# Kernel tuning notes

Hardware: AMD Instinct MI355X
Metric: run time of the kernel (lower is better)

The kernel has to match this reference:

```python
import jax, jax.numpy as jnp
import numpy as np

N_NODES = 50000
N_EDGES = 600000
D_EMB = 128
D_HID = 128
N_HEADS = 4
N_MABS = 7  # ISAB0(mab0,mab1), ISAB1(mab0,mab1), PMA, SAB, SAB
B, S = 16, 512
PROTO = 5


def setup_inputs() -> dict:
    key = jax.random.key(0)
    ks = jax.random.split(key, 24)
    nrm = lambda k, shape, s=0.05: jax.random.normal(k, shape, jnp.float32) * s
    node_embed = nrm(ks[0], (N_NODES + 1, D_EMB), 1.0).at[0].set(0.0)  # padding_idx=0
    return {
        'node_ids': jax.random.randint(ks[1], (B, S), 0, N_NODES),
        'edge_idx': jax.random.randint(ks[2], (2, N_EDGES), 0, N_NODES),
        'edge_attr': jax.random.normal(ks[3], (N_EDGES,), jnp.float32),
        'node_embed': node_embed,
        'lin_W': nrm(ks[4], (D_EMB, D_HID)), 'lin_b': jnp.zeros((D_HID,), jnp.float32),
        'gat_W': nrm(ks[5], (D_HID, D_HID)),
        'gat_att_src': nrm(ks[6], (D_HID,)), 'gat_att_dst': nrm(ks[7], (D_HID,)),
        'gat_bias': jnp.zeros((D_HID,), jnp.float32),
        'mab_Wq': nrm(ks[8], (N_MABS, D_HID, D_HID)), 'mab_bq': jnp.zeros((N_MABS, D_HID), jnp.float32),
        'mab_Wk': nrm(ks[9], (N_MABS, D_HID, D_HID)), 'mab_bk': jnp.zeros((N_MABS, D_HID), jnp.float32),
        'mab_Wv': nrm(ks[10], (N_MABS, D_HID, D_HID)), 'mab_bv': jnp.zeros((N_MABS, D_HID), jnp.float32),
        'mab_Wo': nrm(ks[11], (N_MABS, D_HID, D_HID)), 'mab_bo': jnp.zeros((N_MABS, D_HID), jnp.float32),
        'isab_I': nrm(ks[12], (2, 1, D_HID), 1.0),   # 2 ISAB blocks, num_inds=1
        'pma_S': nrm(ks[13], (1, D_HID), 1.0),       # num_outputs=1 seed
        'dec_W': nrm(ks[14], (D_HID, D_HID)), 'dec_b': jnp.zeros((D_HID,), jnp.float32),
        'prototypes': nrm(ks[15], (1, PROTO, D_HID), 1.0),
    }


def mab(Q, K, Wq, bq, Wk, bk, Wv, bv, Wo, bo):
    # Set-transformer MAB, ln=False; residual uses projected Q; scale by sqrt(full dim)
    D = Q.shape[-1]
    h, d = N_HEADS, D // N_HEADS
    Qp = Q @ Wq + bq
    Kp = K @ Wk + bk
    Vp = K @ Wv + bv
    sh = lambda x: x.reshape(x.shape[0], x.shape[1], h, d).transpose(0, 2, 1, 3)
    A = jax.nn.softmax(jnp.einsum('bhqd,bhkd->bhqk', sh(Qp), sh(Kp)) / np.sqrt(D).astype(np.float32))
    O = sh(Qp) + jnp.einsum('bhqk,bhkd->bhqd', A, sh(Vp))
    O = O.transpose(0, 2, 1, 3).reshape(Q.shape[0], Q.shape[1], D)
    return O + jax.nn.relu(O @ Wo + bo)


def reference(node_ids, edge_idx, edge_attr, node_embed, lin_W, lin_b, gat_W,
              gat_att_src, gat_att_dst, gat_bias, mab_Wq, mab_bq, mab_Wk, mab_bk,
              mab_Wv, mab_bv, mab_Wo, mab_bo, isab_I, pma_S, dec_W, dec_b, prototypes):
    # embed all nodes then linear
    x = node_embed[jnp.arange(N_NODES)] @ lin_W + lin_b          # [N, H]
    # GATConv (1 head, negative_slope=0.2, add_self_loops=True; edge_attr unused)
    loops = jnp.arange(N_NODES)
    src = jnp.concatenate([edge_idx[0], loops])
    dst = jnp.concatenate([edge_idx[1], loops])
    xw = x @ gat_W                                               # [N, H]
    a_s = xw @ gat_att_src                                       # [N]
    a_d = xw @ gat_att_dst
    e = jax.nn.leaky_relu(a_s[src] + a_d[dst], 0.2)              # [E+N]
    m = jax.ops.segment_max(e, dst, num_segments=N_NODES)
    ex = jnp.exp(e - m[dst])
    den = jax.ops.segment_sum(ex, dst, num_segments=N_NODES)
    coef = ex / den[dst]
    x = jax.ops.segment_sum(coef[:, None] * xw[src], dst, num_segments=N_NODES) + gat_bias
    # gather per-sample node sets
    X = x[node_ids]                                              # [B, S, H]
    b = X.shape[0]
    def mb(i, Q, K):
        return mab(Q, K, mab_Wq[i], mab_bq[i], mab_Wk[i], mab_bk[i],
                   mab_Wv[i], mab_bv[i], mab_Wo[i], mab_bo[i])
    # encoder: 2 ISAB blocks (num_inds=1)
    for i in range(2):
        Hb = mb(2 * i, jnp.broadcast_to(isab_I[i][None], (b, 1, D_HID)), X)
        X = mb(2 * i + 1, X, Hb)
    # decoder: PMA -> SAB -> SAB -> Linear
    X = mb(4, jnp.broadcast_to(pma_S[None], (b, 1, D_HID)), X)
    X = mb(5, X, X)
    X = mb(6, X, X)
    X = X @ dec_W + dec_b                                        # [B, 1, H]
    proto = jnp.broadcast_to(prototypes, (b, PROTO, D_HID))
    return jnp.concatenate([X, proto], axis=1)                   # [B, 6, H]
```

## Files before the change

kernel.cpp:

```cpp
#include <hip/hip_runtime.h>
#include <math.h>

#define N_NODES 50000
#define N_EDGES 600000
#define BATCH 16
#define SEQ 512
#define NROWS (BATCH*SEQ)
#define N_ITEMS (N_EDGES + N_NODES)

#define OFF_XW     0L
#define OFF_X      (OFF_XW + 6400000L)
#define OFF_ACC    (OFF_X + 1048576L)
#define OFF_AS     (OFF_ACC + 1048576L)
#define OFF_AD     (OFF_AS + 50000L)
#define OFF_WC     (OFF_AD + 50000L)
#define OFF_BC     (OFF_WC + 16384L)
#define OFF_QP     (OFF_BC + 128L)
#define OFF_WKH    (OFF_QP + 384L)
#define OFF_CKH    (OFF_WKH + 1536L)
#define OFF_VPOD   (OFF_CKH + 16L)
#define OFF_MASK   (OFF_VPOD + 2048L)
#define OFF_DEG    (OFF_MASK + 50000L)
#define OFF_FILL   (OFF_DEG + 8192L)
#define OFF_CNT    (OFF_FILL + 8192L)
#define ZERO_BYTES ((50000L + 8192L + 8192L + 4L) * 4L)
#define OFF_MAP    (OFF_CNT + 4L)
#define OFF_INV    (OFF_MAP + 50000L)
#define OFF_ROWPTR (OFF_INV + 8192L)
#define OFF_COL    (OFF_ROWPTR + 8194L)

__global__ __launch_bounds__(256) void prep_kernel(
    const float* __restrict__ lin_W, const float* __restrict__ lin_b,
    const float* __restrict__ gat_W,
    const float* __restrict__ mab_Wq, const float* __restrict__ mab_bq,
    const float* __restrict__ isab_I, const float* __restrict__ pma_S,
    float* __restrict__ Wc, float* __restrict__ bc, float* __restrict__ qp)
{
    int t = blockIdx.x * 256 + threadIdx.x;
    if (t < 16384) {
        int i = t >> 7, j = t & 127;
        float s = 0.f;
        for (int k = 0; k < 128; ++k) s += lin_W[i*128 + k] * gat_W[k*128 + j];
        Wc[t] = s;
    } else if (t < 16512) {
        int j = t - 16384;
        float s = 0.f;
        for (int k = 0; k < 128; ++k) s += lin_b[k] * gat_W[k*128 + j];
        bc[j] = s;
    } else if (t < 16896) {
        int u = t - 16512;
        int m = u >> 7, c = u & 127;
        int mi = m * 2;
        const float* vec = (m == 0) ? isab_I : (m == 1 ? isab_I + 128 : pma_S);
        float s = mab_bq[mi*128 + c];
        for (int k = 0; k < 128; ++k) s += vec[k] * mab_Wq[mi*16384 + k*128 + c];
        qp[u] = s;
    }
}

__global__ __launch_bounds__(256) void prep2_kernel(
    const float* __restrict__ mab_Wk, const float* __restrict__ mab_bk,
    const float* __restrict__ qp, float* __restrict__ wkh, float* __restrict__ ckh)
{
    int t = blockIdx.x * 256 + threadIdx.x;
    if (t < 1536) {
        int m = t >> 9;
        int h = (t >> 7) & 3;
        int j = t & 127;
        int mi = m * 2;
        const float* Wk = mab_Wk + mi*16384 + j*128 + h*32;
        const float* q  = qp + m*128 + h*32;
        float s = 0.f;
        #pragma unroll
        for (int d = 0; d < 32; ++d) s += Wk[d] * q[d];
        wkh[t] = s;
    } else if (t < 1548) {
        int u = t - 1536;
        int m = u >> 2, h = u & 3;
        int mi = m * 2;
        const float* bk = mab_bk + mi*128 + h*32;
        const float* q  = qp + m*128 + h*32;
        float s = 0.f;
        #pragma unroll
        for (int d = 0; d < 32; ++d) s += bk[d] * q[d];
        ckh[u] = s;
    }
}

__global__ __launch_bounds__(256) void gemm0_kernel(
    const float* __restrict__ Xin, const float* __restrict__ W1,
    const float* __restrict__ b1, float* __restrict__ out1)
{
    __shared__ float Xs[16][128];
    int t = threadIdx.x;
    long row0 = (long)blockIdx.x * 16;
    #pragma unroll
    for (int i = 0; i < 8; ++i) {
        int idx = i*256 + t;
        int r = idx >> 7, k = idx & 127;
        Xs[r][k] = Xin[(row0 + r)*128 + k];
    }
    __syncthreads();
    int c  = t & 127;
    int hh = t >> 7;
    float acc1[8];
    #pragma unroll
    for (int r = 0; r < 8; ++r) acc1[r] = 0.f;
    for (int k4 = 0; k4 < 128; k4 += 4) {
        float xv[8][4];
        #pragma unroll
        for (int r = 0; r < 8; ++r) {
            float4 tmp = *(const float4*)&Xs[hh*8 + r][k4];
            xv[r][0] = tmp.x; xv[r][1] = tmp.y; xv[r][2] = tmp.z; xv[r][3] = tmp.w;
        }
        #pragma unroll
        for (int kk = 0; kk < 4; ++kk) {
            float w1 = W1[(k4 + kk)*128 + c];
            #pragma unroll
            for (int r = 0; r < 8; ++r) acc1[r] += xv[r][kk] * w1;
        }
    }
    float bb = b1[c];
    #pragma unroll
    for (int r = 0; r < 8; ++r) out1[(row0 + hh*8 + r)*128 + c] = acc1[r] + bb;
}

__global__ __launch_bounds__(256) void gemm_odd_kernel(
    const float* __restrict__ X, const float* __restrict__ Wq,
    const float* __restrict__ bq, const float* __restrict__ vpod,
    const float* __restrict__ Wo, const float* __restrict__ bo,
    float* __restrict__ Xout)
{
    __shared__ float Xs[16][128];
    __shared__ float O1[16][128];
    int t = threadIdx.x;
    long row0 = (long)blockIdx.x * 16;
    int bidx = (int)(row0 >> 9);
    #pragma unroll
    for (int i = 0; i < 8; ++i) {
        int idx = i*256 + t;
        int r = idx >> 7, k = idx & 127;
        Xs[r][k] = X[(row0 + r)*128 + k];
    }
    __syncthreads();
    int c  = t & 127;
    int hh = t >> 7;
    float acc[8];
    #pragma unroll
    for (int r = 0; r < 8; ++r) acc[r] = 0.f;
    for (int k4 = 0; k4 < 128; k4 += 4) {
        float xv[8][4];
        #pragma unroll
        for (int r = 0; r < 8; ++r) {
            float4 tmp = *(const float4*)&Xs[hh*8 + r][k4];
            xv[r][0] = tmp.x; xv[r][1] = tmp.y; xv[r][2] = tmp.z; xv[r][3] = tmp.w;
        }
        #pragma unroll
        for (int kk = 0; kk < 4; ++kk) {
            float w = Wq[(k4 + kk)*128 + c];
            #pragma unroll
            for (int r = 0; r < 8; ++r) acc[r] += xv[r][kk] * w;
        }
    }
    float bb = bq[c] + vpod[bidx*128 + c];
    #pragma unroll
    for (int r = 0; r < 8; ++r) O1[hh*8 + r][c] = acc[r] + bb;
    __syncthreads();
    #pragma unroll
    for (int r = 0; r < 8; ++r) acc[r] = 0.f;
    for (int k4 = 0; k4 < 128; k4 += 4) {
        float xv[8][4];
        #pragma unroll
        for (int r = 0; r < 8; ++r) {
            float4 tmp = *(const float4*)&O1[hh*8 + r][k4];
            xv[r][0] = tmp.x; xv[r][1] = tmp.y; xv[r][2] = tmp.z; xv[r][3] = tmp.w;
        }
        #pragma unroll
        for (int kk = 0; kk < 4; ++kk) {
            float w = Wo[(k4 + kk)*128 + c];
            #pragma unroll
            for (int r = 0; r < 8; ++r) acc[r] += xv[r][kk] * w;
        }
    }
    float bb2 = bo[c];
    #pragma unroll
    for (int r = 0; r < 8; ++r)
        Xout[(row0 + hh*8 + r)*128 + c] = O1[hh*8 + r][c] + fmaxf(acc[r] + bb2, 0.f);
}

__global__ __launch_bounds__(256) void avec_kernel(
    const float* __restrict__ xw, const float* __restrict__ att_src,
    const float* __restrict__ att_dst, float* __restrict__ a_s, float* __restrict__ a_d)
{
    int w = threadIdx.x >> 6, lane = threadIdx.x & 63;
    long row = (long)blockIdx.x * 4 + w;
    const float* xr = xw + row*128 + lane*2;
    float x0 = xr[0], x1 = xr[1];
    float s = x0*att_src[lane*2] + x1*att_src[lane*2 + 1];
    float d = x0*att_dst[lane*2] + x1*att_dst[lane*2 + 1];
    #pragma unroll
    for (int off = 32; off > 0; off >>= 1) {
        s += __shfl_down(s, off);
        d += __shfl_down(d, off);
    }
    if (lane == 0) { a_s[row] = s; a_d[row] = d; }
}

__global__ void maskset_kernel(const int* __restrict__ node_ids, int* __restrict__ mask)
{
    int i = blockIdx.x*256 + threadIdx.x;
    if (i < NROWS) mask[node_ids[i]] = 1;
}

__global__ __launch_bounds__(256) void assign_kernel(
    const int* __restrict__ mask, int* __restrict__ map,
    int* __restrict__ inv, int* __restrict__ counter)
{
    __shared__ int wbase[4];
    int i = blockIdx.x*256 + threadIdx.x;
    bool act = (i < N_NODES) && mask[i];
    unsigned long long m = __ballot(act);
    int lane = threadIdx.x & 63;
    int w = threadIdx.x >> 6;
    if (lane == 0) wbase[w] = __popcll(m);
    __syncthreads();
    if (threadIdx.x == 0) {
        int tot = wbase[0] + wbase[1] + wbase[2] + wbase[3];
        int base = atomicAdd(counter, tot);
        int r = base;
        #pragma unroll
        for (int j = 0; j < 4; ++j) { int cj = wbase[j]; wbase[j] = r; r += cj; }
    }
    __syncthreads();
    if (i < N_NODES) {
        int c = -1;
        if (act) {
            c = wbase[w] + __popcll(m & ((1ull << lane) - 1ull));
            inv[c] = i;
        }
        map[i] = c;
    }
}

__global__ __launch_bounds__(256) void pass1_kernel(
    const int* __restrict__ edge_idx, const int* __restrict__ map,
    int* __restrict__ deg)
{
    int i = blockIdx.x*256 + threadIdx.x;
    if (i >= N_ITEMS) return;
    int dd = (i < N_EDGES) ? edge_idx[N_EDGES + i] : i - N_EDGES;
    int c = map[dd];
    if (c >= 0) atomicAdd(&deg[c], 1);
}

__global__ __launch_bounds__(256) void scan_kernel(const int* __restrict__ deg,
                                                   int* __restrict__ rowptr)
{
    __shared__ int part[256];
    __shared__ int pref[256];
    int t = threadIdx.x;
    int base = t * 32;
    int s = 0;
    #pragma unroll
    for (int j = 0; j < 32; ++j) s += deg[base + j];
    part[t] = s;
    __syncthreads();
    if (t == 0) {
        int run = 0;
        for (int i = 0; i < 256; ++i) { pref[i] = run; run += part[i]; }
    }
    __syncthreads();
    int run = pref[t];
    #pragma unroll
    for (int j = 0; j < 32; ++j) { rowptr[base + j] = run; run += deg[base + j]; }
    if (t == 255) rowptr[8192] = run;
}

__global__ __launch_bounds__(256) void pass2_kernel(
    const int* __restrict__ edge_idx, const int* __restrict__ map,
    const int* __restrict__ rowptr, int* __restrict__ fill,
    int* __restrict__ colx)
{
    int i = blockIdx.x*256 + threadIdx.x;
    if (i >= N_ITEMS) return;
    int s, dd;
    if (i < N_EDGES) { s = edge_idx[i]; dd = edge_idx[N_EDGES + i]; }
    else             { s = dd = i - N_EDGES; }
    int c = map[dd];
    if (c < 0) return;
    int pos = rowptr[c] + atomicAdd(&fill[c], 1);
    colx[pos] = s;
}

__global__ __launch_bounds__(256) void agg_kernel(
    const int* __restrict__ rowptr, const int* __restrict__ colx,
    const int* __restrict__ inv, const int* __restrict__ cnt,
    const float* __restrict__ a_s, const float* __restrict__ a_d,
    const float* __restrict__ xw, float* __restrict__ acc)
{
    int c = blockIdx.x*4 + (threadIdx.x >> 6);
    int lane = threadIdx.x & 63;
    if (c >= *cnt) return;
    int dd = inv[c];
    float ad = a_d[dd];
    int beg = rowptr[c], end = rowptr[c + 1];
    float s0 = 0.f, s1 = 0.f, den = 0.f;
    for (int j = beg; j < end; ++j) {
        int s = colx[j];
        float e = a_s[s] + ad;
        e = (e > 0.f) ? e : 0.2f * e;
        float ex = __expf(e);
        den += ex;
        float2 v = *(const float2*)(xw + (long)s*128 + lane*2);
        s0 += ex * v.x;
        s1 += ex * v.y;
    }
    float inv_d = 1.f / den;
    float* o = acc + (long)c*128 + lane*2;
    o[0] = s0 * inv_d;
    o[1] = s1 * inv_d;
}

__global__ __launch_bounds__(256) void gather_kernel(
    const int* __restrict__ node_ids, const int* __restrict__ map,
    const float* __restrict__ acc, const float* __restrict__ gat_bias,
    float* __restrict__ X)
{
    int w = threadIdx.x >> 6, lane = threadIdx.x & 63;
    int j = blockIdx.x*4 + w;
    int c = map[node_ids[j]];
    const float2 v = *(const float2*)(acc + (long)c*128 + lane*2);
    float* o = X + (long)j*128 + lane*2;
    o[0] = v.x + gat_bias[lane*2];
    o[1] = v.y + gat_bias[lane*2 + 1];
}

__device__ __forceinline__ float matvec_qs(
    const float* __restrict__ W, const float* xs, float (*red)[128], int t)
{
    int c = t & 127, q = t >> 7;
    float acc = 0.f;
    #pragma unroll
    for (int j = 0; j < 32; ++j) {
        int k = q*32 + j;
        acc += xs[k] * W[k*128 + c];
    }
    red[q][c] = acc;
    __syncthreads();
    float s = 0.f;
    if (t < 128) s = red[0][t] + red[1][t] + red[2][t] + red[3][t];
    __syncthreads();
    return s;
}

__global__ __launch_bounds__(512) void attn_even_kernel(
    const float* __restrict__ X, const float* __restrict__ qp,
    const float* __restrict__ wkh, const float* __restrict__ ckh,
    const float* __restrict__ Wv, const float* __restrict__ bv,
    const float* __restrict__ Wo, const float* __restrict__ bo,
    const float* __restrict__ Wv1, const float* __restrict__ bv1,
    float* __restrict__ vpod)
{
    __shared__ float l_sm[4][512];
    __shared__ float part[4][4][128];
    __shared__ float wks[4][128];
    __shared__ float u_sm[4][128];
    __shared__ float red[4][128];
    __shared__ float red64[4][64];
    __shared__ float mx[4], dn[4];
    __shared__ float qs[128], Ovec[128], Hsm[128];
    int b = blockIdx.x, t = threadIdx.x;
    if (t < 128) qs[t] = qp[t];
    wks[t >> 7][t & 127] = wkh[t];
    __syncthreads();
    const float scale = 0.088388347648318447f;
    float ck0 = ckh[0], ck1 = ckh[1], ck2 = ckh[2], ck3 = ckh[3];
    {
        const float* xr = X + ((long)b*512 + t)*128;
        float l[4] = {0.f, 0.f, 0.f, 0.f};
        for (int d4 = 0; d4 < 128; d4 += 4) {
            float4 xv = *(const float4*)&xr[d4];
            #pragma unroll
            for (int h = 0; h < 4; ++h)
                l[h] += xv.x*wks[h][d4] + xv.y*wks[h][d4+1]
                      + xv.z*wks[h][d4+2] + xv.w*wks[h][d4+3];
        }
        l_sm[0][t] = (l[0] + ck0) * scale;
        l_sm[1][t] = (l[1] + ck1) * scale;
        l_sm[2][t] = (l[2] + ck2) * scale;
        l_sm[3][t] = (l[3] + ck3) * scale;
    }
    __syncthreads();
    if (t < 256) {
        int h = t >> 6, i = t & 63;
        float m = -1e30f;
        #pragma unroll
        for (int j = 0; j < 8; ++j) m = fmaxf(m, l_sm[h][i + 64*j]);
        red64[h][i] = m;
    }
    __syncthreads();
    if (t < 4) {
        float m = -1e30f;
        for (int i = 0; i < 64; ++i) m = fmaxf(m, red64[t][i]);
        mx[t] = m;
    }
    __syncthreads();
    #pragma unroll
    for (int h = 0; h < 4; ++h) l_sm[h][t] = __expf(l_sm[h][t] - mx[h]);
    __syncthreads();
    if (t < 256) {
        int h = t >> 6, i = t & 63;
        float ssum = 0.f;
        #pragma unroll
        for (int j = 0; j < 8; ++j) ssum += l_sm[h][i + 64*j];
        red64[h][i] = ssum;
    }
    __syncthreads();
    if (t < 4) {
        float sm = 0.f;
        for (int i = 0; i < 64; ++i) sm += red64[t][i];
        dn[t] = 1.f / sm;
    }
    __syncthreads();
    {
        int q4 = t >> 7, d = t & 127;
        float a0 = 0.f, a1 = 0.f, a2 = 0.f, a3 = 0.f;
        const float* xc = X + ((long)b*512 + q4*128)*128 + d;
        for (int kk = 0; kk < 128; ++kk) {
            float xv = xc[(long)kk*128];
            int k = q4*128 + kk;
            a0 += xv * l_sm[0][k];
            a1 += xv * l_sm[1][k];
            a2 += xv * l_sm[2][k];
            a3 += xv * l_sm[3][k];
        }
        part[q4][0][d] = a0; part[q4][1][d] = a1; part[q4][2][d] = a2; part[q4][3][d] = a3;
    }
    __syncthreads();
    {
        int h = t >> 7, d = t & 127;
        u_sm[h][d] = (part[0][h][d] + part[1][h][d] + part[2][h][d] + part[3][h][d]) * dn[h];
    }
    __syncthreads();
    {
        int q4 = t >> 7, c = t & 127, h = c >> 5;
        float a = 0.f;
        #pragma unroll
        for (int j = 0; j < 32; ++j) {
            int k = q4*32 + j;
            a += u_sm[h][k] * Wv[k*128 + c];
        }
        red[q4][c] = a;
    }
    __syncthreads();
    if (t < 128) Ovec[t] = qs[t] + red[0][t] + red[1][t] + red[2][t] + red[3][t] + bv[t];
    __syncthreads();
    float mv = matvec_qs(Wo, Ovec, red, t);
    if (t < 128) Hsm[t] = Ovec[t] + fmaxf(mv + bo[t], 0.f);
    __syncthreads();
    float mv2 = matvec_qs(Wv1, Hsm, red, t);
    if (t < 128) vpod[b*128 + t] = mv2 + bv1[t];
}

__global__ __launch_bounds__(512) void attn_pma_kernel(
    const float* __restrict__ X, const float* __restrict__ qp,
    const float* __restrict__ wkh, const float* __restrict__ ckh,
    const float* __restrict__ mab_Wq, const float* __restrict__ mab_bq,
    const float* __restrict__ mab_Wv, const float* __restrict__ mab_bv,
    const float* __restrict__ mab_Wo, const float* __restrict__ mab_bo,
    const float* __restrict__ dec_W, const float* __restrict__ dec_b,
    const float* __restrict__ protos, float* __restrict__ out)
{
    __shared__ float l_sm[4][512];
    __shared__ float part[4][4][128];
    __shared__ float wks[4][128];
    __shared__ float u_sm[4][128];
    __shared__ float red[4][128];
    __shared__ float red64[4][64];
    __shared__ float mx[4], dn[4];
    __shared__ float qs[128], Ovec[128], S1[128], S2[128];
    int b = blockIdx.x, t = threadIdx.x;
    if (t < 128) qs[t] = qp[t];
    wks[t >> 7][t & 127] = wkh[t];
    __syncthreads();
    const float scale = 0.088388347648318447f;
    float ck0 = ckh[0], ck1 = ckh[1], ck2 = ckh[2], ck3 = ckh[3];
    {
        const float* xr = X + ((long)b*512 + t)*128;
        float l[4] = {0.f, 0.f, 0.f, 0.f};
        for (int d4 = 0; d4 < 128; d4 += 4) {
            float4 xv = *(const float4*)&xr[d4];
            #pragma unroll
            for (int h = 0; h < 4; ++h)
                l[h] += xv.x*wks[h][d4] + xv.y*wks[h][d4+1]
                      + xv.z*wks[h][d4+2] + xv.w*wks[h][d4+3];
        }
        l_sm[0][t] = (l[0] + ck0) * scale;
        l_sm[1][t] = (l[1] + ck1) * scale;
        l_sm[2][t] = (l[2] + ck2) * scale;
        l_sm[3][t] = (l[3] + ck3) * scale;
    }
    __syncthreads();
    if (t < 256) {
        int h = t >> 6, i = t & 63;
        float m = -1e30f;
        #pragma unroll
        for (int j = 0; j < 8; ++j) m = fmaxf(m, l_sm[h][i + 64*j]);
        red64[h][i] = m;
    }
    __syncthreads();
    if (t < 4) {
        float m = -1e30f;
        for (int i = 0; i < 64; ++i) m = fmaxf(m, red64[t][i]);
        mx[t] = m;
    }
    __syncthreads();
    #pragma unroll
    for (int h = 0; h < 4; ++h) l_sm[h][t] = __expf(l_sm[h][t] - mx[h]);
    __syncthreads();
    if (t < 256) {
        int h = t >> 6, i = t & 63;
        float ssum = 0.f;
        #pragma unroll
        for (int j = 0; j < 8; ++j) ssum += l_sm[h][i + 64*j];
        red64[h][i] = ssum;
    }
    __syncthreads();
    if (t < 4) {
        float sm = 0.f;
        for (int i = 0; i < 64; ++i) sm += red64[t][i];
        dn[t] = 1.f / sm;
    }
    __syncthreads();
    {
        int q4 = t >> 7, d = t & 127;
        float a0 = 0.f, a1 = 0.f, a2 = 0.f, a3 = 0.f;
        const float* xc = X + ((long)b*512 + q4*128)*128 + d;
        for (int kk = 0; kk < 128; ++kk) {
            float xv = xc[(long)kk*128];
            int k = q4*128 + kk;
            a0 += xv * l_sm[0][k];
            a1 += xv * l_sm[1][k];
            a2 += xv * l_sm[2][k];
            a3 += xv * l_sm[3][k];
        }
        part[q4][0][d] = a0; part[q4][1][d] = a1; part[q4][2][d] = a2; part[q4][3][d] = a3;
    }
    __syncthreads();
    {
        int h = t >> 7, d = t & 127;
        u_sm[h][d] = (part[0][h][d] + part[1][h][d] + part[2][h][d] + part[3][h][d]) * dn[h];
    }
    __syncthreads();
    {
        int q4 = t >> 7, c = t & 127, h = c >> 5;
        float a = 0.f;
        #pragma unroll
        for (int j = 0; j < 32; ++j) {
            int k = q4*32 + j;
            a += u_sm[h][k] * (mab_Wv + 4*16384)[k*128 + c];
        }
        red[q4][c] = a;
    }
    __syncthreads();
    if (t < 128) Ovec[t] = qs[t] + red[0][t] + red[1][t] + red[2][t] + red[3][t]
                         + mab_bv[4*128 + t];
    __syncthreads();
    float mv = matvec_qs(mab_Wo + 4*16384, Ovec, red, t);
    if (t < 128) S1[t] = Ovec[t] + fmaxf(mv + mab_bo[4*128 + t], 0.f);
    __syncthreads();
    float q5 = matvec_qs(mab_Wq + 5*16384, S1, red, t);
    float v5 = matvec_qs(mab_Wv + 5*16384, S1, red, t);
    if (t < 128) S2[t] = q5 + mab_bq[5*128 + t] + v5 + mab_bv[5*128 + t];
    __syncthreads();
    float m5 = matvec_qs(mab_Wo + 5*16384, S2, red, t);
    if (t < 128) S1[t] = S2[t] + fmaxf(m5 + mab_bo[5*128 + t], 0.f);
    __syncthreads();
    float q6 = matvec_qs(mab_Wq + 6*16384, S1, red, t);
    float v6 = matvec_qs(mab_Wv + 6*16384, S1, red, t);
    if (t < 128) S2[t] = q6 + mab_bq[6*128 + t] + v6 + mab_bv[6*128 + t];
    __syncthreads();
    float m6 = matvec_qs(mab_Wo + 6*16384, S2, red, t);
    if (t < 128) S1[t] = S2[t] + fmaxf(m6 + mab_bo[6*128 + t], 0.f);
    __syncthreads();
    float y = matvec_qs(dec_W, S1, red, t);
    if (t < 128) out[b*768 + t] = y + dec_b[t];
    {
        int p = t >> 7, c = t & 127;
        out[b*768 + (1 + p)*128 + c] = protos[p*128 + c];
        if (t < 128) out[b*768 + 640 + t] = protos[512 + t];
    }
}

extern "C" void kernel_launch(void* const* d_in, const int* in_sizes, int n_in,
                              void* d_out, int out_size, void* d_ws, size_t ws_size,
                              hipStream_t stream)
{
    (void)in_sizes; (void)n_in; (void)out_size; (void)ws_size;
    const int*   node_ids  = (const int*)d_in[0];
    const int*   edge_idx  = (const int*)d_in[1];
    const float* node_embed= (const float*)d_in[3];
    const float* lin_W     = (const float*)d_in[4];
    const float* lin_b     = (const float*)d_in[5];
    const float* gat_W     = (const float*)d_in[6];
    const float* att_src   = (const float*)d_in[7];
    const float* att_dst   = (const float*)d_in[8];
    const float* gat_bias  = (const float*)d_in[9];
    const float* mab_Wq    = (const float*)d_in[10];
    const float* mab_bq    = (const float*)d_in[11];
    const float* mab_Wk    = (const float*)d_in[12];
    const float* mab_bk    = (const float*)d_in[13];
    const float* mab_Wv    = (const float*)d_in[14];
    const float* mab_bv    = (const float*)d_in[15];
    const float* mab_Wo    = (const float*)d_in[16];
    const float* mab_bo    = (const float*)d_in[17];
    const float* isab_I    = (const float*)d_in[18];
    const float* pma_S     = (const float*)d_in[19];
    const float* dec_W     = (const float*)d_in[20];
    const float* dec_b     = (const float*)d_in[21];
    const float* protos    = (const float*)d_in[22];

    float* ws    = (float*)d_ws;
    float* xw    = ws + OFF_XW;
    float* X     = ws + OFF_X;
    float* acc   = ws + OFF_ACC;
    float* a_s   = ws + OFF_AS;
    float* a_d   = ws + OFF_AD;
    float* Wc    = ws + OFF_WC;
    float* bc    = ws + OFF_BC;
    float* qp    = ws + OFF_QP;
    float* wkh   = ws + OFF_WKH;
    float* ckh   = ws + OFF_CKH;
    float* vpod  = ws + OFF_VPOD;
    int*   mask  = (int*)(ws + OFF_MASK);
    int*   deg   = (int*)(ws + OFF_DEG);
    int*   fill  = (int*)(ws + OFF_FILL);
    int*   cnt   = (int*)(ws + OFF_CNT);
    int*   map   = (int*)(ws + OFF_MAP);
    int*   inv   = (int*)(ws + OFF_INV);
    int*   rowp  = (int*)(ws + OFF_ROWPTR);
    int*   colx  = (int*)(ws + OFF_COL);
    float* out   = (float*)d_out;

    hipMemsetAsync(ws + OFF_MASK, 0, ZERO_BYTES, stream);

    prep_kernel<<<66, 256, 0, stream>>>(lin_W, lin_b, gat_W, mab_Wq, mab_bq, isab_I, pma_S,
                                        Wc, bc, qp);
    prep2_kernel<<<7, 256, 0, stream>>>(mab_Wk, mab_bk, qp, wkh, ckh);
    gemm0_kernel<<<N_NODES/16, 256, 0, stream>>>(node_embed, Wc, bc, xw);
    avec_kernel<<<N_NODES/4, 256, 0, stream>>>(xw, att_src, att_dst, a_s, a_d);
    maskset_kernel<<<(NROWS + 255)/256, 256, 0, stream>>>(node_ids, mask);
    assign_kernel<<<(N_NODES + 255)/256, 256, 0, stream>>>(mask, map, inv, cnt);
    pass1_kernel<<<(N_ITEMS + 255)/256, 256, 0, stream>>>(edge_idx, map, deg);
    scan_kernel<<<1, 256, 0, stream>>>(deg, rowp);
    pass2_kernel<<<(N_ITEMS + 255)/256, 256, 0, stream>>>(edge_idx, map, rowp, fill, colx);
    agg_kernel<<<NROWS/4, 256, 0, stream>>>(rowp, colx, inv, cnt, a_s, a_d, xw, acc);
    gather_kernel<<<NROWS/4, 256, 0, stream>>>(node_ids, map, acc, gat_bias, X);

    for (int i = 0; i < 2; ++i) {
        int o = 2*i + 1;
        attn_even_kernel<<<16, 512, 0, stream>>>(X, qp + i*128, wkh + i*512, ckh + i*4,
                                                 mab_Wv + (2*i)*16384, mab_bv + (2*i)*128,
                                                 mab_Wo + (2*i)*16384, mab_bo + (2*i)*128,
                                                 mab_Wv + o*16384, mab_bv + o*128,
                                                 vpod);
        gemm_odd_kernel<<<NROWS/16, 256, 0, stream>>>(X, mab_Wq + o*16384, mab_bq + o*128,
                                                      vpod, mab_Wo + o*16384, mab_bo + o*128,
                                                      X);
    }
    attn_pma_kernel<<<16, 512, 0, stream>>>(X, qp + 256, wkh + 1024, ckh + 8,
                                            mab_Wq, mab_bq, mab_Wv, mab_bv, mab_Wo, mab_bo,
                                            dec_W, dec_b, protos, out);
}
```

Measured before the change: 318.6 us.

## Aggregate raw embeddings before the linear projection to shrink the node GEMM

```diff
diff --git a/kernel.cpp b/kernel.cpp
--- a/kernel.cpp
+++ b/kernel.cpp
@@ -8,18 +8,22 @@
 #define NROWS (BATCH*SEQ)
 #define N_ITEMS (N_EDGES + N_NODES)
 
-#define OFF_XW     0L
-#define OFF_X      (OFF_XW + 6400000L)
-#define OFF_ACC    (OFF_X + 1048576L)
-#define OFF_AS     (OFF_ACC + 1048576L)
-#define OFF_AD     (OFF_AS + 50000L)
-#define OFF_WC     (OFF_AD + 50000L)
-#define OFF_BC     (OFF_WC + 16384L)
-#define OFF_QP     (OFF_BC + 128L)
-#define OFF_WKH    (OFF_QP + 384L)
-#define OFF_CKH    (OFF_WKH + 1536L)
-#define OFF_VPOD   (OFF_CKH + 16L)
-#define OFF_MASK   (OFF_VPOD + 2048L)
+#define OFF_X      0L
+#define OFF_ACC    1048576L
+#define OFF_X2     2097152L
+#define OFF_AS     3145728L
+#define OFF_AD     3195728L
+#define OFF_WC     3245728L
+#define OFF_BC     3262112L
+#define OFF_QP     3262240L
+#define OFF_WKH    3262624L
+#define OFF_CKH    3264160L
+#define OFF_VAS    3264176L
+#define OFF_VAD    3264304L
+#define OFF_BFIN   3264432L
+#define OFF_CSD    3264560L
+#define OFF_VPOD   3264564L
+#define OFF_MASK   3266612L
 #define OFF_DEG    (OFF_MASK + 50000L)
 #define OFF_FILL   (OFF_DEG + 8192L)
 #define OFF_CNT    (OFF_FILL + 8192L)
@@ -60,7 +64,12 @@
 
 __global__ __launch_bounds__(256) void prep2_kernel(
     const float* __restrict__ mab_Wk, const float* __restrict__ mab_bk,
-    const float* __restrict__ qp, float* __restrict__ wkh, float* __restrict__ ckh)
+    const float* __restrict__ qp, const float* __restrict__ Wc,
+    const float* __restrict__ bc, const float* __restrict__ att_src,
+    const float* __restrict__ att_dst, const float* __restrict__ gat_bias,
+    float* __restrict__ wkh, float* __restrict__ ckh,
+    float* __restrict__ vas, float* __restrict__ vad,
+    float* __restrict__ bfin, float* __restrict__ csd)
 {
     int t = blockIdx.x * 256 + threadIdx.x;
     if (t < 1536) {
@@ -84,6 +93,27 @@
         #pragma unroll
         for (int d = 0; d < 32; ++d) s += bk[d] * q[d];
         ckh[u] = s;
+    } else if (t < 1676) {
+        int k = t - 1548;
+        float s = 0.f;
+        for (int j = 0; j < 128; ++j) s += Wc[k*128 + j] * att_src[j];
+        vas[k] = s;
+    } else if (t < 1804) {
+        int k = t - 1676;
+        float s = 0.f;
+        for (int j = 0; j < 128; ++j) s += Wc[k*128 + j] * att_dst[j];
+        vad[k] = s;
+    } else if (t < 1932) {
+        int j = t - 1804;
+        bfin[j] = bc[j] + gat_bias[j];
+    } else if (t == 1932) {
+        float s = 0.f;
+        for (int j = 0; j < 128; ++j) s += bc[j] * att_src[j];
+        csd[0] = s;
+    } else if (t == 1933) {
+        float s = 0.f;
+        for (int j = 0; j < 128; ++j) s += bc[j] * att_dst[j];
+        csd[1] = s;
     }
 }
 
@@ -189,21 +219,22 @@
 }
 
 __global__ __launch_bounds__(256) void avec_kernel(
-    const float* __restrict__ xw, const float* __restrict__ att_src,
-    const float* __restrict__ att_dst, float* __restrict__ a_s, float* __restrict__ a_d)
+    const float* __restrict__ embed, const float* __restrict__ vas,
+    const float* __restrict__ vad, const float* __restrict__ csd,
+    float* __restrict__ a_s, float* __restrict__ a_d)
 {
     int w = threadIdx.x >> 6, lane = threadIdx.x & 63;
     long row = (long)blockIdx.x * 4 + w;
-    const float* xr = xw + row*128 + lane*2;
+    const float* xr = embed + row*128 + lane*2;
     float x0 = xr[0], x1 = xr[1];
-    float s = x0*att_src[lane*2] + x1*att_src[lane*2 + 1];
-    float d = x0*att_dst[lane*2] + x1*att_dst[lane*2 + 1];
+    float s = x0*vas[lane*2] + x1*vas[lane*2 + 1];
+    float d = x0*vad[lane*2] + x1*vad[lane*2 + 1];
     #pragma unroll
     for (int off = 32; off > 0; off >>= 1) {
         s += __shfl_down(s, off);
         d += __shfl_down(d, off);
     }
-    if (lane == 0) { a_s[row] = s; a_d[row] = d; }
+    if (lane == 0) { a_s[row] = s + csd[0]; a_d[row] = d + csd[1]; }
 }
 
 __global__ void maskset_kernel(const int* __restrict__ node_ids, int* __restrict__ mask)
@@ -296,7 +327,7 @@
     const int* __restrict__ rowptr, const int* __restrict__ colx,
     const int* __restrict__ inv, const int* __restrict__ cnt,
     const float* __restrict__ a_s, const float* __restrict__ a_d,
-    const float* __restrict__ xw, float* __restrict__ acc)
+    const float* __restrict__ embed, float* __restrict__ acc)
 {
     int c = blockIdx.x*4 + (threadIdx.x >> 6);
     int lane = threadIdx.x & 63;
@@ -311,7 +342,7 @@
         e = (e > 0.f) ? e : 0.2f * e;
         float ex = __expf(e);
         den += ex;
-        float2 v = *(const float2*)(xw + (long)s*128 + lane*2);
+        float2 v = *(const float2*)(embed + (long)s*128 + lane*2);
         s0 += ex * v.x;
         s1 += ex * v.y;
     }
@@ -323,16 +354,13 @@
 
 __global__ __launch_bounds__(256) void gather_kernel(
     const int* __restrict__ node_ids, const int* __restrict__ map,
-    const float* __restrict__ acc, const float* __restrict__ gat_bias,
-    float* __restrict__ X)
+    const float* __restrict__ X2, float* __restrict__ X)
 {
     int w = threadIdx.x >> 6, lane = threadIdx.x & 63;
     int j = blockIdx.x*4 + w;
     int c = map[node_ids[j]];
-    const float2 v = *(const float2*)(acc + (long)c*128 + lane*2);
-    float* o = X + (long)j*128 + lane*2;
-    o[0] = v.x + gat_bias[lane*2];
-    o[1] = v.y + gat_bias[lane*2 + 1];
+    const float2 v = *(const float2*)(X2 + (long)c*128 + lane*2);
+    *(float2*)(X + (long)j*128 + lane*2) = v;
 }
 
 __device__ __forceinline__ float matvec_qs(
@@ -621,9 +649,9 @@
     const float* protos    = (const float*)d_in[22];
 
     float* ws    = (float*)d_ws;
-    float* xw    = ws + OFF_XW;
     float* X     = ws + OFF_X;
     float* acc   = ws + OFF_ACC;
+    float* X2    = ws + OFF_X2;
     float* a_s   = ws + OFF_AS;
     float* a_d   = ws + OFF_AD;
     float* Wc    = ws + OFF_WC;
@@ -631,6 +659,10 @@
     float* qp    = ws + OFF_QP;
     float* wkh   = ws + OFF_WKH;
     float* ckh   = ws + OFF_CKH;
+    float* vas   = ws + OFF_VAS;
+    float* vad   = ws + OFF_VAD;
+    float* bfin  = ws + OFF_BFIN;
+    float* csd   = ws + OFF_CSD;
     float* vpod  = ws + OFF_VPOD;
     int*   mask  = (int*)(ws + OFF_MASK);
     int*   deg   = (int*)(ws + OFF_DEG);
@@ -646,16 +678,17 @@
 
     prep_kernel<<<66, 256, 0, stream>>>(lin_W, lin_b, gat_W, mab_Wq, mab_bq, isab_I, pma_S,
                                         Wc, bc, qp);
-    prep2_kernel<<<7, 256, 0, stream>>>(mab_Wk, mab_bk, qp, wkh, ckh);
-    gemm0_kernel<<<N_NODES/16, 256, 0, stream>>>(node_embed, Wc, bc, xw);
-    avec_kernel<<<N_NODES/4, 256, 0, stream>>>(xw, att_src, att_dst, a_s, a_d);
+    prep2_kernel<<<8, 256, 0, stream>>>(mab_Wk, mab_bk, qp, Wc, bc, att_src, att_dst, gat_bias,
+                                        wkh, ckh, vas, vad, bfin, csd);
+    avec_kernel<<<N_NODES/4, 256, 0, stream>>>(node_embed, vas, vad, csd, a_s, a_d);
     maskset_kernel<<<(NROWS + 255)/256, 256, 0, stream>>>(node_ids, mask);
     assign_kernel<<<(N_NODES + 255)/256, 256, 0, stream>>>(mask, map, inv, cnt);
     pass1_kernel<<<(N_ITEMS + 255)/256, 256, 0, stream>>>(edge_idx, map, deg);
     scan_kernel<<<1, 256, 0, stream>>>(deg, rowp);
     pass2_kernel<<<(N_ITEMS + 255)/256, 256, 0, stream>>>(edge_idx, map, rowp, fill, colx);
-    agg_kernel<<<NROWS/4, 256, 0, stream>>>(rowp, colx, inv, cnt, a_s, a_d, xw, acc);
-    gather_kernel<<<NROWS/4, 256, 0, stream>>>(node_ids, map, acc, gat_bias, X);
+    agg_kernel<<<NROWS/4, 256, 0, stream>>>(rowp, colx, inv, cnt, a_s, a_d, node_embed, acc);
+    gemm0_kernel<<<NROWS/16, 256, 0, stream>>>(acc, Wc, bfin, X2);
+    gather_kernel<<<NROWS/4, 256, 0, stream>>>(node_ids, map, X2, X);
 
     for (int i = 0; i < 2; ++i) {
         int o = 2*i + 1;
```

After: 290.5 us. 8.8% less time.
